# Performance work log

Hardware: AMD Instinct MI355X
Metric: run time of the kernel (lower is better)

## Reference

```python
import jax, jax.numpy as jnp
import numpy as np

B, S, D = 2, 2048, 2048
RANK = 512
N_HEADS = 16
DROPOUT_RATE = 0.1
KEEP = 1.0 - DROPOUT_RATE  # original safe_dropout scales by 1/keep even when deterministic


def setup_inputs() -> dict:
    key = jax.random.key(0)
    ks = jax.random.split(key, 9)
    return {
        "x": jax.random.normal(ks[0], (B, S, D), jnp.float32),
        "g_Q": jax.random.uniform(ks[1], (B, S, RANK), jnp.float32),
        "g_K": jax.random.uniform(ks[2], (B, S, RANK), jnp.float32),
        "g_V": jax.random.uniform(ks[3], (B, S, RANK), jnp.float32),
        "qk_read": jax.random.normal(ks[4], (RANK, D), jnp.float32) * 0.02,
        "qk_write": jax.random.normal(ks[5], (RANK, D), jnp.float32) * 0.02,
        "v_read": jax.random.normal(ks[6], (RANK, D), jnp.float32) * 0.02,
        "v_write": jax.random.normal(ks[7], (RANK, D), jnp.float32) * 0.02,
        "W_O": jax.random.normal(ks[8], (D, D), jnp.float32) * 0.02,
    }


def _gated_lowrank(x, g, rd, wr):
    # g * (x @ rd.T) @ wr : [B,S,D] -> [B,S,rank] -> [B,S,D]
    return (g * jnp.einsum('bsd,rd->bsr', x, rd)) @ wr


def reference(x, g_Q, g_K, g_V, qk_read, qk_write, v_read, v_write, W_O):
    Bx, Sx, Dx = x.shape
    d_head = Dx // N_HEADS

    Q = _gated_lowrank(x, g_Q, qk_read, qk_write)
    K = _gated_lowrank(x, g_K, qk_read, qk_write)
    V = _gated_lowrank(x, g_V, v_read, v_write)

    Q = Q.reshape(Bx, Sx, N_HEADS, d_head).transpose(0, 2, 1, 3)
    K = K.reshape(Bx, Sx, N_HEADS, d_head).transpose(0, 2, 1, 3)
    V = V.reshape(Bx, Sx, N_HEADS, d_head).transpose(0, 2, 1, 3)

    scale = jnp.sqrt(jnp.float32(d_head))
    scores = jnp.einsum('bhsd,bhtd->bhst', Q, K) / scale  # [B,H,S,S]
    causal = jnp.tril(jnp.ones((Sx, Sx), dtype=jnp.bool_))
    scores = jnp.where(causal, scores, jnp.finfo(scores.dtype).min)
    attn_w = jax.nn.softmax(scores, axis=-1)
    attn_w = attn_w / KEEP  # deterministic branch of original safe_dropout

    out = jnp.einsum('bhst,bhtd->bhsd', attn_w, V)
    out = out.transpose(0, 2, 1, 3).reshape(Bx, Sx, Dx)
    out = out @ W_O
    out = out / KEEP  # deterministic dropout scaling
    return out
```

## Files before the change

### kernel.cpp

```cpp
#include <hip/hip_runtime.h>
#include <cstdint>
#include <cstddef>

typedef unsigned short u16;
typedef unsigned int u32;
typedef __attribute__((ext_vector_type(4))) float f32x4;
typedef __attribute__((ext_vector_type(8))) __bf16 bf16x8;
typedef __attribute__((ext_vector_type(8))) u16 u16x8;
typedef __attribute__((ext_vector_type(4))) u16 u16x4;
typedef __attribute__((ext_vector_type(2))) u32 u32x2;

__device__ __forceinline__ u16 f2bf(float x) {
  u32 u = __builtin_bit_cast(u32, x);
  u += 0x7fffu + ((u >> 16) & 1u);
  return (u16)(u >> 16);
}
__device__ __forceinline__ float bf2f(u16 b) {
  return __builtin_bit_cast(float, (u32)b << 16);
}
__device__ __forceinline__ bf16x8 ldfrag(const u16* p) {
  return __builtin_bit_cast(bf16x8, *(const u16x8*)p);
}
__device__ __forceinline__ void gload_lds16(const void* g, void* l) {
  auto gp = (const __attribute__((address_space(1))) u32*)g;
  auto lp = (__attribute__((address_space(3))) u32*)l;
  __builtin_amdgcn_global_load_lds(gp, lp, 16, 0, 0);
}
#define MFMA16(a, b, c) __builtin_amdgcn_mfma_f32_16x16x32_bf16(a, b, c, 0, 0, 0)

__global__ void prep_kernel(const float* __restrict__ x, const float* __restrict__ qkr,
                            const float* __restrict__ vr, const float* __restrict__ qkw,
                            const float* __restrict__ vw, const float* __restrict__ wo,
                            u16* __restrict__ x_bf, u16* __restrict__ qkr_b,
                            u16* __restrict__ vr_b, u16* __restrict__ qkwT,
                            u16* __restrict__ vwT, u16* __restrict__ woT) {
  __shared__ float tile[32][33];
  const int bid = blockIdx.x;
  const int tid = threadIdx.x;
  if (bid < 10240) {
    const float* in;
    u16* out;
    int base;
    if (bid < 8192) { in = x; out = x_bf; base = bid; }
    else if (bid < 9216) { in = qkr; out = qkr_b; base = bid - 8192; }
    else { in = vr; out = vr_b; base = bid - 9216; }
    int i = base * 1024 + tid * 4;
    f32x4 v = *(const f32x4*)(in + i);
    u16x4 r = { f2bf(v[0]), f2bf(v[1]), f2bf(v[2]), f2bf(v[3]) };
    *(u16x4*)(out + i) = r;
  } else {
    const float* in;
    u16* out;
    int R, C, local;
    if (bid < 11264) { in = qkw; out = qkwT; R = 512; C = 2048; local = bid - 10240; }
    else if (bid < 12288) { in = vw; out = vwT; R = 512; C = 2048; local = bid - 11264; }
    else { in = wo; out = woT; R = 2048; C = 2048; local = bid - 12288; }
    int bx = (local & 63) * 32, by = (local >> 6) * 32;
    int tx = tid & 31, ty = tid >> 5;
#pragma unroll
    for (int i = 0; i < 32; i += 8)
      tile[ty + i][tx] = in[(size_t)(by + ty + i) * C + bx + tx];
    __syncthreads();
#pragma unroll
    for (int i = 0; i < 32; i += 8)
      out[(size_t)(bx + ty + i) * R + by + tx] = f2bf(tile[tx][ty + i]);
  }
}

template <bool F32OUT>
__device__ __forceinline__ void gemm_body(const u16* __restrict__ A,
                                          const u16* __restrict__ Bt,
                                          void* __restrict__ Cp, int N, int K,
                                          float scale, size_t bm, size_t bn,
                                          u16* Al, u16* Bl) {
  const int tid = threadIdx.x;
  const int lane = tid & 63;
  const int w = tid >> 6;
  const int wr = (w >> 1) * 64;
  const int wc = (w & 1) * 64;

  f32x4 acc[4][4] = {};

  const int srow = lane >> 2;
  const int sch = lane & 3;
  const int kc = lane >> 4;
  const int rl = lane & 15;

  for (int kt = 0; kt < K; kt += 32) {
#pragma unroll
    for (int half = 0; half < 2; ++half) {
      int rb = half * 64 + w * 16;
      int row = rb + srow;
      int ch = sch ^ ((row >> 1) & 3);
      gload_lds16(A + (bm + row) * (size_t)K + kt + ch * 8, &Al[rb * 32]);
    }
#pragma unroll
    for (int half = 0; half < 2; ++half) {
      int rb = half * 64 + w * 16;
      int row = rb + srow;
      int ch = sch ^ ((row >> 1) & 3);
      gload_lds16(Bt + (bn + row) * (size_t)K + kt + ch * 8, &Bl[rb * 32]);
    }
    asm volatile("s_waitcnt vmcnt(0)" ::: "memory");
    __syncthreads();

    bf16x8 af[4], bfr[4];
#pragma unroll
    for (int m = 0; m < 4; ++m) {
      int row = wr + m * 16 + rl;
      af[m] = ldfrag(&Al[row * 32 + (kc ^ ((row >> 1) & 3)) * 8]);
    }
#pragma unroll
    for (int n = 0; n < 4; ++n) {
      int row = wc + n * 16 + rl;
      bfr[n] = ldfrag(&Bl[row * 32 + (kc ^ ((row >> 1) & 3)) * 8]);
    }
#pragma unroll
    for (int m = 0; m < 4; ++m)
#pragma unroll
      for (int n = 0; n < 4; ++n)
        acc[m][n] = MFMA16(af[m], bfr[n], acc[m][n]);
    __syncthreads();
  }

  const int r0 = (lane >> 4) * 4;
#pragma unroll
  for (int m = 0; m < 4; ++m) {
    size_t grow = bm + wr + m * 16 + r0;
#pragma unroll
    for (int n = 0; n < 4; ++n) {
      size_t gcol = bn + wc + n * 16 + rl;
#pragma unroll
      for (int r = 0; r < 4; ++r) {
        float v = acc[m][n][r] * scale;
        if constexpr (F32OUT)
          ((float*)Cp)[(grow + r) * (size_t)N + gcol] = v;
        else
          ((u16*)Cp)[(grow + r) * (size_t)N + gcol] = f2bf(v);
      }
    }
  }
}

template <bool F32OUT>
__global__ void gemm_bt(const u16* __restrict__ A, const u16* __restrict__ Bt,
                        void* __restrict__ Cp, int N, int K, float scale) {
  __shared__ u16 Al[128 * 32];
  __shared__ u16 Bl[128 * 32];
  gemm_body<F32OUT>(A, Bt, Cp, N, K, scale, (size_t)blockIdx.y * 128,
                    (size_t)blockIdx.x * 128, Al, Bl);
}

__global__ void gemm_qkv(const u16* __restrict__ Acat, const u16* __restrict__ qkwT,
                         u16* __restrict__ Qb, const u16* __restrict__ vwT,
                         const u16* __restrict__ Av, u16* __restrict__ Vt) {
  __shared__ u16 Al[128 * 32];
  __shared__ u16 Bl[128 * 32];
  const int bid = blockIdx.x;
  if (bid < 1024) {
    gemm_body<false>(Acat, qkwT, Qb, 2048, 512, 1.f, (size_t)(bid >> 4) * 128,
                     (size_t)(bid & 15) * 128, Al, Bl);
  } else {
    const int l = bid - 1024;
    gemm_body<false>(vwT, Av, Vt, 4096, 512, 1.f, (size_t)(l >> 5) * 128,
                     (size_t)(l & 31) * 128, Al, Bl);
  }
}

__global__ void gemm_gate(const u16* __restrict__ A, const u16* __restrict__ Bt,
                          const float* __restrict__ gq, const float* __restrict__ gk,
                          const float* __restrict__ gv, u16* __restrict__ Aq,
                          u16* __restrict__ Ak, u16* __restrict__ Av, int K) {
  __shared__ u16 Al[128 * 32];
  __shared__ u16 Bl[128 * 32];
  const float SC = 0.1275255128608411f;
  const int tid = threadIdx.x;
  const int lane = tid & 63;
  const int w = tid >> 6;
  const int wr = (w >> 1) * 64;
  const int wc = (w & 1) * 64;
  const size_t bm = (size_t)blockIdx.y * 128;
  const size_t bn = (size_t)blockIdx.x * 128;

  f32x4 acc[4][4] = {};

  const int srow = lane >> 2;
  const int sch = lane & 3;
  const int kc = lane >> 4;
  const int rl = lane & 15;

  for (int kt = 0; kt < K; kt += 32) {
#pragma unroll
    for (int half = 0; half < 2; ++half) {
      int rb = half * 64 + w * 16;
      int row = rb + srow;
      int ch = sch ^ ((row >> 1) & 3);
      gload_lds16(A + (bm + row) * (size_t)K + kt + ch * 8, &Al[rb * 32]);
    }
#pragma unroll
    for (int half = 0; half < 2; ++half) {
      int rb = half * 64 + w * 16;
      int row = rb + srow;
      int ch = sch ^ ((row >> 1) & 3);
      gload_lds16(Bt + (bn + row) * (size_t)K + kt + ch * 8, &Bl[rb * 32]);
    }
    asm volatile("s_waitcnt vmcnt(0)" ::: "memory");
    __syncthreads();

    bf16x8 af[4], bfr[4];
#pragma unroll
    for (int m = 0; m < 4; ++m) {
      int row = wr + m * 16 + rl;
      af[m] = ldfrag(&Al[row * 32 + (kc ^ ((row >> 1) & 3)) * 8]);
    }
#pragma unroll
    for (int n = 0; n < 4; ++n) {
      int row = wc + n * 16 + rl;
      bfr[n] = ldfrag(&Bl[row * 32 + (kc ^ ((row >> 1) & 3)) * 8]);
    }
#pragma unroll
    for (int m = 0; m < 4; ++m)
#pragma unroll
      for (int n = 0; n < 4; ++n)
        acc[m][n] = MFMA16(af[m], bfr[n], acc[m][n]);
    __syncthreads();
  }

  const int r0 = (lane >> 4) * 4;
  const bool phalf = (bn < 512);
#pragma unroll
  for (int m = 0; m < 4; ++m) {
    size_t grow = bm + wr + m * 16 + r0;
#pragma unroll
    for (int n = 0; n < 4; ++n) {
      size_t gcol = bn + wc + n * 16 + rl;
#pragma unroll
      for (int r = 0; r < 4; ++r) {
        float v = acc[m][n][r];
        if (phalf) {
          size_t idx = (grow + r) * 512 + gcol;
          Aq[idx] = f2bf(gq[idx] * SC * v);
          Ak[idx] = f2bf(gk[idx] * v);
        } else {
          size_t idx = (grow + r) * 512 + (gcol - 512);
          Av[idx] = f2bf(gv[idx] * v);
        }
      }
    }
  }
}

__global__ __launch_bounds__(256, 3) void attn_kernel(const u16* __restrict__ Q,
                                                      const u16* __restrict__ Kg,
                                                      const u16* __restrict__ Vt,
                                                      u16* __restrict__ AO) {
  __shared__ u16 Kl[2][64 * 128];
  __shared__ u16 Vl[128 * 64];

  const int tid = threadIdx.x;
  const int lane = tid & 63;
  const int w = tid >> 6;
  const int bh = blockIdx.x;
  const int qb = 31 - blockIdx.y;
  const int b = bh >> 4;
  const int h = bh & 15;

  const int rl = lane & 15;
  const int g4 = lane >> 4;

  const float THR = 10.0f;

  bf16x8 ones;
  {
    u16x8 ou;
#pragma unroll
    for (int j = 0; j < 8; ++j) ou[j] = 0x3F80;
    ones = __builtin_bit_cast(bf16x8, ou);
  }

  auto stageK = [&](int buf, int t0) {
    int roff = lane >> 4;
    int cch = lane & 15;
#pragma unroll
    for (int i = 0; i < 4; ++i) {
      int rb = w * 16 + i * 4;
      int row = rb + roff;
      int ch = cch ^ (row & 7);
      gload_lds16(Kg + ((size_t)b * 2048 + t0 + row) * 2048 + h * 128 + ch * 8,
                  &Kl[buf][rb * 128]);
    }
  };
  auto stageV = [&](int t0) {
    int roff = lane >> 3;
    int cch = lane & 7;
#pragma unroll
    for (int i = 0; i < 4; ++i) {
      int rb = w * 32 + i * 8;
      int row = rb + roff;
      int ch = cch ^ (row & 7);
      gload_lds16(Vt + (size_t)(h * 128 + row) * 4096 + (size_t)b * 2048 + t0 + ch * 8,
                  &Vl[rb * 64]);
    }
  };

  const int ntiles = qb + 1;
  const int qq = qb * 64 + w * 16 + rl;
  const size_t qrow0 = (size_t)b * 2048 + (size_t)qb * 64;

  bf16x8 qf[4];
  {
    const u16* qp = Q + (qrow0 + w * 16 + rl) * 2048 + h * 128 + g4 * 8;
#pragma unroll
    for (int ks = 0; ks < 4; ++ks) qf[ks] = ldfrag(qp + ks * 32);
  }

  float m_r = -3.0e38f;
  float l_r[4];
#pragma unroll
  for (int r = 0; r < 4; ++r) l_r[r] = 0.f;
  f32x4 oacc[8] = {};

  stageK(0, 0);
  __syncthreads();
  int cur = 0;

#pragma unroll 1
  for (int t = 0; t < ntiles; ++t) {
    const int t0 = t * 64;
    stageV(t0);
    const bool pref = (t + 1 < ntiles);
    if (pref) stageK(cur ^ 1, (t + 1) * 64);

    float p[4][4];
    __builtin_amdgcn_s_setprio(1);
#pragma unroll
    for (int nf = 0; nf < 4; ++nf) {
      f32x4 c = {};
      int trow = nf * 16 + rl;
#pragma unroll
      for (int ks = 0; ks < 4; ++ks) {
        bf16x8 kf = ldfrag(&Kl[cur][trow * 128 + ((ks * 4 + g4) ^ (trow & 7)) * 8]);
        c = MFMA16(kf, qf[ks], c);
      }
      if (t == qb) {
        int tb = t0 + nf * 16 + g4 * 4;
#pragma unroll
        for (int r = 0; r < 4; ++r)
          p[nf][r] = (tb + r <= qq) ? c[r] : -3.0e38f;
      } else {
#pragma unroll
        for (int r = 0; r < 4; ++r) p[nf][r] = c[r];
      }
    }
    __builtin_amdgcn_s_setprio(0);

    float mx = p[0][0];
#pragma unroll
    for (int nf = 0; nf < 4; ++nf)
#pragma unroll
      for (int r = 0; r < 4; ++r) mx = fmaxf(mx, p[nf][r]);
    mx = fmaxf(mx, __shfl_xor(mx, 16));
    mx = fmaxf(mx, __shfl_xor(mx, 32));

    if (__any(mx - m_r > THR)) {
      float mn = fmaxf(m_r, mx);
      float alpha = exp2f(m_r - mn);
      m_r = mn;
#pragma unroll
      for (int r = 0; r < 4; ++r) {
        float av = __shfl(alpha, g4 * 4 + r, 16);
        l_r[r] *= av;
#pragma unroll
        for (int nf = 0; nf < 8; ++nf) oacc[nf][r] *= av;
      }
    }

    u32x2 pk[4];
#pragma unroll
    for (int nf = 0; nf < 4; ++nf) {
      u32 e0 = __builtin_bit_cast(u32, exp2f(p[nf][0] - m_r));
      u32 e1 = __builtin_bit_cast(u32, exp2f(p[nf][1] - m_r));
      u32 e2 = __builtin_bit_cast(u32, exp2f(p[nf][2] - m_r));
      u32 e3 = __builtin_bit_cast(u32, exp2f(p[nf][3] - m_r));
      pk[nf][0] = (e1 & 0xffff0000u) | (e0 >> 16);
      pk[nf][1] = (e3 & 0xffff0000u) | (e2 >> 16);
    }

    if (pref) asm volatile("s_waitcnt vmcnt(4)\n\ts_barrier" ::: "memory");
    else      asm volatile("s_waitcnt vmcnt(0)\n\ts_barrier" ::: "memory");

    u16* pl = &Kl[cur][w * 1024];
#pragma unroll
    for (int nf = 0; nf < 4; ++nf) {
      int c8 = ((nf * 2 + (g4 >> 1)) ^ (rl & 7)) * 8 + (g4 & 1) * 4;
      *(u32x2*)(&pl[rl * 64 + c8]) = pk[nf];
    }

    __builtin_amdgcn_s_setprio(1);
    f32x4 rs = {};
#pragma unroll
    for (int ks = 0; ks < 2; ++ks) {
      bf16x8 pa = ldfrag(&pl[rl * 64 + ((ks * 4 + g4) ^ (rl & 7)) * 8]);
#pragma unroll
      for (int nf = 0; nf < 8; ++nf) {
        int drow = nf * 16 + rl;
        bf16x8 vf = ldfrag(&Vl[drow * 64 + ((ks * 4 + g4) ^ (drow & 7)) * 8]);
        oacc[nf] = MFMA16(pa, vf, oacc[nf]);
      }
      rs = MFMA16(pa, ones, rs);
    }
    __builtin_amdgcn_s_setprio(0);
#pragma unroll
    for (int r = 0; r < 4; ++r) l_r[r] += rs[r];

    __syncthreads();
    cur ^= 1;
  }

#pragma unroll
  for (int nf = 0; nf < 8; ++nf) {
    size_t dc = (size_t)h * 128 + nf * 16 + rl;
#pragma unroll
    for (int r = 0; r < 4; ++r) {
      float v = oacc[nf][r] / l_r[r];
      AO[(qrow0 + w * 16 + g4 * 4 + r) * 2048 + dc] = f2bf(v);
    }
  }
}


extern "C" void kernel_launch(void* const* d_in, const int* in_sizes, int n_in,
                              void* d_out, int out_size, void* d_ws, size_t ws_size,
                              hipStream_t stream) {
  const float* x = (const float*)d_in[0];
  const float* gQ = (const float*)d_in[1];
  const float* gK = (const float*)d_in[2];
  const float* gV = (const float*)d_in[3];
  const float* qkr = (const float*)d_in[4];
  const float* qkw = (const float*)d_in[5];
  const float* vr = (const float*)d_in[6];
  const float* vw = (const float*)d_in[7];
  const float* wo = (const float*)d_in[8];
  float* out = (float*)d_out;

  u16* p = (u16*)d_ws;
  u16* x_bf = p;   p += 8388608;
  u16* qkr_b = p;  p += 1048576;
  u16* vr_b = p;   p += 1048576;
  u16* qkwT = p;   p += 1048576;
  u16* vwT = p;    p += 1048576;
  u16* woT = p;    p += 4194304;
  u16* Aq = p;     p += 2097152;
  u16* Ak = p;     p += 2097152;
  u16* Av = p;     p += 2097152;
  u16* Qb = p;     p += 8388608;
  u16* Kb = p;     p += 8388608;
  u16* Vt = x_bf;
  u16* AO = Qb;

  prep_kernel<<<16384, 256, 0, stream>>>(x, qkr, vr, qkw, vw, wo,
                                         x_bf, qkr_b, vr_b, qkwT, vwT, woT);

  gemm_gate<<<dim3(8, 32), 256, 0, stream>>>(x_bf, qkr_b, gQ, gK, gV, Aq, Ak, Av, 2048);

  gemm_qkv<<<1536, 256, 0, stream>>>(Aq, qkwT, Qb, vwT, Av, Vt);

  attn_kernel<<<dim3(32, 32), 256, 0, stream>>>(Qb, Kb, Vt, AO);

  gemm_bt<true><<<dim3(16, 32), 256, 0, stream>>>(AO, woT, out, 2048, 2048,
                                                  1.2345679012345678f);
}
```

Baseline: 221.9 us.

## Double-buffer LDS in shared GEMM mainloop and halve gate GEMM N-tile

Result: faster. 210.0 us (median of 3 runs) (-5.4%).

```diff
diff --git a/kernel.cpp b/kernel.cpp
--- a/kernel.cpp
+++ b/kernel.cpp
@@ -67,68 +67,93 @@
   }
 }
 
-template <bool F32OUT>
-__device__ __forceinline__ void gemm_body(const u16* __restrict__ A,
+template <int BM, int BN>
+__device__ __forceinline__ void gemm_main(const u16* __restrict__ A,
                                           const u16* __restrict__ Bt,
-                                          void* __restrict__ Cp, int N, int K,
-                                          float scale, size_t bm, size_t bn,
-                                          u16* Al, u16* Bl) {
+                                          int K, size_t bm, size_t bn,
+                                          u16* Al, u16* Bl,
+                                          f32x4 (&acc)[BM / 32][BN / 32]) {
   const int tid = threadIdx.x;
   const int lane = tid & 63;
   const int w = tid >> 6;
-  const int wr = (w >> 1) * 64;
-  const int wc = (w & 1) * 64;
-
-  f32x4 acc[4][4] = {};
-
+  const int wr = (w >> 1) * (BM / 2);
+  const int wc = (w & 1) * (BN / 2);
   const int srow = lane >> 2;
   const int sch = lane & 3;
   const int kc = lane >> 4;
   const int rl = lane & 15;
-
-  for (int kt = 0; kt < K; kt += 32) {
-#pragma unroll
-    for (int half = 0; half < 2; ++half) {
-      int rb = half * 64 + w * 16;
+  constexpr int ASZ = BM * 32;
+  constexpr int BSZ = BN * 32;
+
+  auto stage = [&](int buf, int kt) {
+#pragma unroll
+    for (int i = 0; i < BM / 64; ++i) {
+      int rb = w * 16 + i * 64;
       int row = rb + srow;
       int ch = sch ^ ((row >> 1) & 3);
-      gload_lds16(A + (bm + row) * (size_t)K + kt + ch * 8, &Al[rb * 32]);
-    }
-#pragma unroll
-    for (int half = 0; half < 2; ++half) {
-      int rb = half * 64 + w * 16;
+      gload_lds16(A + (bm + row) * (size_t)K + kt + ch * 8, &Al[buf * ASZ + rb * 32]);
+    }
+#pragma unroll
+    for (int i = 0; i < BN / 64; ++i) {
+      int rb = w * 16 + i * 64;
       int row = rb + srow;
       int ch = sch ^ ((row >> 1) & 3);
-      gload_lds16(Bt + (bn + row) * (size_t)K + kt + ch * 8, &Bl[rb * 32]);
-    }
+      gload_lds16(Bt + (bn + row) * (size_t)K + kt + ch * 8, &Bl[buf * BSZ + rb * 32]);
+    }
+  };
+
+  stage(0, 0);
+  asm volatile("s_waitcnt vmcnt(0)" ::: "memory");
+  __syncthreads();
+  int cur = 0;
+
+  for (int kt = 0; kt < K; kt += 32) {
+    if (kt + 32 < K) stage(cur ^ 1, kt + 32);
+
+    bf16x8 af[BM / 32], bfr[BN / 32];
+#pragma unroll
+    for (int m = 0; m < BM / 32; ++m) {
+      int row = wr + m * 16 + rl;
+      af[m] = ldfrag(&Al[cur * ASZ + row * 32 + (kc ^ ((row >> 1) & 3)) * 8]);
+    }
+#pragma unroll
+    for (int n = 0; n < BN / 32; ++n) {
+      int row = wc + n * 16 + rl;
+      bfr[n] = ldfrag(&Bl[cur * BSZ + row * 32 + (kc ^ ((row >> 1) & 3)) * 8]);
+    }
+#pragma unroll
+    for (int m = 0; m < BM / 32; ++m)
+#pragma unroll
+      for (int n = 0; n < BN / 32; ++n)
+        acc[m][n] = MFMA16(af[m], bfr[n], acc[m][n]);
+
     asm volatile("s_waitcnt vmcnt(0)" ::: "memory");
     __syncthreads();
-
-    bf16x8 af[4], bfr[4];
-#pragma unroll
-    for (int m = 0; m < 4; ++m) {
-      int row = wr + m * 16 + rl;
-      af[m] = ldfrag(&Al[row * 32 + (kc ^ ((row >> 1) & 3)) * 8]);
-    }
-#pragma unroll
-    for (int n = 0; n < 4; ++n) {
-      int row = wc + n * 16 + rl;
-      bfr[n] = ldfrag(&Bl[row * 32 + (kc ^ ((row >> 1) & 3)) * 8]);
-    }
-#pragma unroll
-    for (int m = 0; m < 4; ++m)
-#pragma unroll
-      for (int n = 0; n < 4; ++n)
-        acc[m][n] = MFMA16(af[m], bfr[n], acc[m][n]);
-    __syncthreads();
-  }
-
+    cur ^= 1;
+  }
+}
+
+template <bool F32OUT, int BM, int BN>
+__global__ void gemm_bt(const u16* __restrict__ A, const u16* __restrict__ Bt,
+                        void* __restrict__ Cp, int N, int K, float scale) {
+  __shared__ u16 Al[2 * BM * 32];
+  __shared__ u16 Bl[2 * BN * 32];
+  const int lane = threadIdx.x & 63;
+  const int w = threadIdx.x >> 6;
+  const size_t bm = (size_t)blockIdx.y * BM;
+  const size_t bn = (size_t)blockIdx.x * BN;
+  f32x4 acc[BM / 32][BN / 32] = {};
+  gemm_main<BM, BN>(A, Bt, K, bm, bn, Al, Bl, acc);
+
+  const int wr = (w >> 1) * (BM / 2);
+  const int wc = (w & 1) * (BN / 2);
+  const int rl = lane & 15;
   const int r0 = (lane >> 4) * 4;
 #pragma unroll
-  for (int m = 0; m < 4; ++m) {
+  for (int m = 0; m < BM / 32; ++m) {
     size_t grow = bm + wr + m * 16 + r0;
 #pragma unroll
-    for (int n = 0; n < 4; ++n) {
+    for (int n = 0; n < BN / 32; ++n) {
       size_t gcol = bn + wc + n * 16 + rl;
 #pragma unroll
       for (int r = 0; r < 4; ++r) {
@@ -142,28 +167,44 @@
   }
 }
 
-template <bool F32OUT>
-__global__ void gemm_bt(const u16* __restrict__ A, const u16* __restrict__ Bt,
-                        void* __restrict__ Cp, int N, int K, float scale) {
-  __shared__ u16 Al[128 * 32];
-  __shared__ u16 Bl[128 * 32];
-  gemm_body<F32OUT>(A, Bt, Cp, N, K, scale, (size_t)blockIdx.y * 128,
-                    (size_t)blockIdx.x * 128, Al, Bl);
-}
-
 __global__ void gemm_qkv(const u16* __restrict__ Acat, const u16* __restrict__ qkwT,
                          u16* __restrict__ Qb, const u16* __restrict__ vwT,
                          const u16* __restrict__ Av, u16* __restrict__ Vt) {
-  __shared__ u16 Al[128 * 32];
-  __shared__ u16 Bl[128 * 32];
+  __shared__ u16 Al[2 * 128 * 32];
+  __shared__ u16 Bl[2 * 128 * 32];
   const int bid = blockIdx.x;
+  const int lane = threadIdx.x & 63;
+  const int w = threadIdx.x >> 6;
+  const u16 *A, *Bt;
+  u16* C;
+  size_t bm, bn;
+  int N;
   if (bid < 1024) {
-    gemm_body<false>(Acat, qkwT, Qb, 2048, 512, 1.f, (size_t)(bid >> 4) * 128,
-                     (size_t)(bid & 15) * 128, Al, Bl);
+    A = Acat; Bt = qkwT; C = Qb; N = 2048;
+    bm = (size_t)(bid >> 4) * 128;
+    bn = (size_t)(bid & 15) * 128;
   } else {
-    const int l = bid - 1024;
-    gemm_body<false>(vwT, Av, Vt, 4096, 512, 1.f, (size_t)(l >> 5) * 128,
-                     (size_t)(l & 31) * 128, Al, Bl);
+    A = vwT; Bt = Av; C = Vt; N = 4096;
+    bm = (size_t)((bid - 1024) >> 5) * 128;
+    bn = (size_t)((bid - 1024) & 31) * 128;
+  }
+  f32x4 acc[4][4] = {};
+  gemm_main<128, 128>(A, Bt, 512, bm, bn, Al, Bl, acc);
+
+  const int wr = (w >> 1) * 64;
+  const int wc = (w & 1) * 64;
+  const int rl = lane & 15;
+  const int r0 = (lane >> 4) * 4;
+#pragma unroll
+  for (int m = 0; m < 4; ++m) {
+    size_t grow = bm + wr + m * 16 + r0;
+#pragma unroll
+    for (int n = 0; n < 4; ++n) {
+      size_t gcol = bn + wc + n * 16 + rl;
+#pragma unroll
+      for (int r = 0; r < 4; ++r)
+        C[(grow + r) * (size_t)N + gcol] = f2bf(acc[m][n][r]);
+    }
   }
 }
 
@@ -171,68 +212,26 @@
                           const float* __restrict__ gq, const float* __restrict__ gk,
                           const float* __restrict__ gv, u16* __restrict__ Aq,
                           u16* __restrict__ Ak, u16* __restrict__ Av, int K) {
-  __shared__ u16 Al[128 * 32];
-  __shared__ u16 Bl[128 * 32];
+  __shared__ u16 Al[2 * 128 * 32];
+  __shared__ u16 Bl[2 * 64 * 32];
   const float SC = 0.1275255128608411f;
-  const int tid = threadIdx.x;
-  const int lane = tid & 63;
-  const int w = tid >> 6;
+  const int lane = threadIdx.x & 63;
+  const int w = threadIdx.x >> 6;
+  const size_t bm = (size_t)blockIdx.y * 128;
+  const size_t bn = (size_t)blockIdx.x * 64;
+  f32x4 acc[4][2] = {};
+  gemm_main<128, 64>(A, Bt, K, bm, bn, Al, Bl, acc);
+
   const int wr = (w >> 1) * 64;
-  const int wc = (w & 1) * 64;
-  const size_t bm = (size_t)blockIdx.y * 128;
-  const size_t bn = (size_t)blockIdx.x * 128;
-
-  f32x4 acc[4][4] = {};
-
-  const int srow = lane >> 2;
-  const int sch = lane & 3;
-  const int kc = lane >> 4;
+  const int wc = (w & 1) * 32;
   const int rl = lane & 15;
-
-  for (int kt = 0; kt < K; kt += 32) {
-#pragma unroll
-    for (int half = 0; half < 2; ++half) {
-      int rb = half * 64 + w * 16;
-      int row = rb + srow;
-      int ch = sch ^ ((row >> 1) & 3);
-      gload_lds16(A + (bm + row) * (size_t)K + kt + ch * 8, &Al[rb * 32]);
-    }
-#pragma unroll
-    for (int half = 0; half < 2; ++half) {
-      int rb = half * 64 + w * 16;
-      int row = rb + srow;
-      int ch = sch ^ ((row >> 1) & 3);
-      gload_lds16(Bt + (bn + row) * (size_t)K + kt + ch * 8, &Bl[rb * 32]);
-    }
-    asm volatile("s_waitcnt vmcnt(0)" ::: "memory");
-    __syncthreads();
-
-    bf16x8 af[4], bfr[4];
-#pragma unroll
-    for (int m = 0; m < 4; ++m) {
-      int row = wr + m * 16 + rl;
-      af[m] = ldfrag(&Al[row * 32 + (kc ^ ((row >> 1) & 3)) * 8]);
-    }
-#pragma unroll
-    for (int n = 0; n < 4; ++n) {
-      int row = wc + n * 16 + rl;
-      bfr[n] = ldfrag(&Bl[row * 32 + (kc ^ ((row >> 1) & 3)) * 8]);
-    }
-#pragma unroll
-    for (int m = 0; m < 4; ++m)
-#pragma unroll
-      for (int n = 0; n < 4; ++n)
-        acc[m][n] = MFMA16(af[m], bfr[n], acc[m][n]);
-    __syncthreads();
-  }
-
   const int r0 = (lane >> 4) * 4;
   const bool phalf = (bn < 512);
 #pragma unroll
   for (int m = 0; m < 4; ++m) {
     size_t grow = bm + wr + m * 16 + r0;
 #pragma unroll
-    for (int n = 0; n < 4; ++n) {
+    for (int n = 0; n < 2; ++n) {
       size_t gcol = bn + wc + n * 16 + rl;
 #pragma unroll
       for (int r = 0; r < 4; ++r) {
@@ -461,12 +460,12 @@
   prep_kernel<<<16384, 256, 0, stream>>>(x, qkr, vr, qkw, vw, wo,
                                          x_bf, qkr_b, vr_b, qkwT, vwT, woT);
 
-  gemm_gate<<<dim3(8, 32), 256, 0, stream>>>(x_bf, qkr_b, gQ, gK, gV, Aq, Ak, Av, 2048);
+  gemm_gate<<<dim3(16, 32), 256, 0, stream>>>(x_bf, qkr_b, gQ, gK, gV, Aq, Ak, Av, 2048);
 
   gemm_qkv<<<1536, 256, 0, stream>>>(Aq, qkwT, Qb, vwT, Av, Vt);
 
   attn_kernel<<<dim3(32, 32), 256, 0, stream>>>(Qb, Kb, Vt, AO);
 
-  gemm_bt<true><<<dim3(16, 32), 256, 0, stream>>>(AO, woT, out, 2048, 2048,
-                                                  1.2345679012345678f);
-}
+  gemm_bt<true, 128, 128><<<dim3(16, 32), 256, 0, stream>>>(AO, woT, out, 2048, 2048,
+                                                            1.2345679012345678f);
+}
```
